# Kernel tuning notes

Hardware: AMD Instinct MI355X
Metric: run time of the kernel (lower is better)

Reference implementation:

```python
import jax, jax.numpy as jnp
import numpy as np

B, C, L = 1, 256, 1024      # batch, channels, seq_length
WIN, FEAT = 80, 256          # window_size, feature_size


def setup_inputs() -> dict:
    key = jax.random.key(0)
    ks = jax.random.split(key, 9)
    s = 0.02
    return {
        "x":  jax.random.normal(ks[0], (B, C, L), dtype=jnp.float32),
        # weights stored as [in, out] (transpose of torch Linear.weight)
        "Wq": jax.random.normal(ks[1], (WIN, FEAT), dtype=jnp.float32) * s,
        "bq": jax.random.normal(ks[2], (FEAT,), dtype=jnp.float32) * s,
        "Wk": jax.random.normal(ks[3], (WIN, FEAT), dtype=jnp.float32) * s,
        "bk": jax.random.normal(ks[4], (FEAT,), dtype=jnp.float32) * s,
        "Wv": jax.random.normal(ks[5], (WIN, FEAT), dtype=jnp.float32) * s,
        "bv": jax.random.normal(ks[6], (FEAT,), dtype=jnp.float32) * s,
        "Wf": jax.random.normal(ks[7], (FEAT, C), dtype=jnp.float32) * s,
        "bf": jax.random.normal(ks[8], (C,), dtype=jnp.float32) * s,
    }


def reference(x, Wq, bq, Wk, bk, Wv, bv, Wf, bf):
    Bb, Cc, Ll = x.shape
    half = WIN // 2
    # fixed-width window per position, clamped to stay in-bounds
    starts = jnp.clip(jnp.arange(Ll) - half, 0, Ll - WIN)          # [L]
    idx = starts[:, None] + jnp.arange(WIN)                        # [L, W]
    win = x[:, :, idx]                                             # [B, C, L, W]
    win = win.transpose(0, 2, 1, 3)                                # [B, L, C, W]
    q = win @ Wq + bq                                              # [B, L, C, F]
    k = win @ Wk + bk                                              # [B, L, C, F]
    v = win @ Wv + bv                                              # [B, L, C, F]
    scores = jax.nn.softmax(jnp.einsum('blcf,bldf->blcd', q, k), axis=-1)  # [B,L,C,C]
    attn = jnp.einsum('blcd,bldf->blcf', scores, v)                # [B, L, C, F]
    pooled = attn.mean(axis=2)                                     # [B, L, F] (mean over channels)
    out = pooled @ Wf + bf                                         # [B, L, C]
    return out.transpose(0, 2, 1)                                  # [B, C, L]
```

## Files before the change

### kernel.cpp

```cpp
#include <hip/hip_runtime.h>

#define Lc    1024
#define Cc    256
#define WINc  80
#define FEATc 256
#define RS    104
#define KP    96

typedef __attribute__((ext_vector_type(8))) short bf16x8;
typedef __attribute__((ext_vector_type(8))) unsigned short u16x8;
typedef __attribute__((ext_vector_type(4))) float f32x4;

__device__ inline unsigned short f2bf(float f) {
    unsigned int u = __float_as_uint(f);
    unsigned int r = u + 0x7FFFu + ((u >> 16) & 1u);
    return (unsigned short)(r >> 16);
}
__device__ inline float bf2f(unsigned short h) {
    return __uint_as_float(((unsigned int)h) << 16);
}

__global__ __launch_bounds__(128) void precompute_kernel(
    const float* __restrict__ Wq, const float* __restrict__ bq,
    const float* __restrict__ Wk,
    unsigned short* __restrict__ Gtb)
{
    const int t = blockIdx.x;
    const int w = threadIdx.x;
    if (w >= RS) return;
    float acc = 0.f;
    if (t < WINc && w < WINc) {
        for (int f = 0; f < FEATc; ++f)
            acc = fmaf(Wq[w * FEATc + f], Wk[t * FEATc + f], acc);
    } else if (t == WINc && w < WINc) {
        for (int f = 0; f < FEATc; ++f)
            acc = fmaf(bq[f], Wk[w * FEATc + f], acc);
    }
    Gtb[t * RS + w] = f2bf(acc);
}

__global__ __launch_bounds__(1024, 4) void local_attn_kernel(
    const float* __restrict__ x,
    const float* __restrict__ Wv, const float* __restrict__ bv,
    const float* __restrict__ Wf, const float* __restrict__ bf,
    const unsigned short* __restrict__ Gt_ws,
    float* __restrict__ out)
{
    __shared__ unsigned short winb[Cc * RS];
    __shared__ unsigned short Tb[Cc * RS];
    __shared__ unsigned short Gtb[KP * RS];
    __shared__ float sbeta[Cc];
    __shared__ float scratch[16 * Cc];
    __shared__ float sbar[Cc];
    __shared__ float ubuf[WINc];
    __shared__ float pooled[FEATc];

    const int l = blockIdx.x;
    int s = l - WINc / 2;
    s = s < 0 ? 0 : (s > (Lc - WINc) ? (Lc - WINc) : s);
    const int tid  = threadIdx.x;
    const int lane = tid & 63;
    const int wid  = tid >> 6;
    const int lr   = lane & 15;
    const int lkq  = lane >> 4;

    for (int i = tid; i < Cc * WINc / 8; i += 1024) {
        const int c  = i / 10;
        const int j8 = (i - c * 10) * 8;
        const float* xp = &x[c * Lc + s + j8];
        u16x8 v;
        #pragma unroll
        for (int e = 0; e < 8; ++e) v[e] = f2bf(xp[e]);
        *(u16x8*)&winb[c * RS + j8] = v;
    }
    for (int i = tid; i < Cc * 8; i += 1024) {
        const int c = i >> 3, j = i & 7;
        *(unsigned int*)&winb[c * RS + WINc + 2 * j] = 0u;
    }
    for (int i = tid; i < KP * RS / 2; i += 1024)
        ((unsigned int*)Gtb)[i] = ((const unsigned int*)Gt_ws)[i];
    __syncthreads();

    {
        const int arow = wid * 16 + lr;
        #pragma unroll
        for (int nt = 0; nt < 6; ++nt) {
            f32x4 acc = {0.f, 0.f, 0.f, 0.f};
            #pragma unroll
            for (int kc = 0; kc < 3; ++kc) {
                const int ko = kc * 32 + lkq * 8;
                bf16x8 a = *(const bf16x8*)&winb[arow * RS + ko];
                bf16x8 b = *(const bf16x8*)&Gtb[(nt * 16 + lr) * RS + ko];
                acc = __builtin_amdgcn_mfma_f32_16x16x32_bf16(a, b, acc, 0, 0, 0);
            }
            const int orow = wid * 16 + lkq * 4;
            const int ocol = nt * 16 + lr;
            #pragma unroll
            for (int r = 0; r < 4; ++r)
                Tb[(orow + r) * RS + ocol] = f2bf(acc[r]);
            if (nt == 5 && lr == 0) {
                #pragma unroll
                for (int r = 0; r < 4; ++r) sbeta[orow + r] = acc[r];
            }
        }
    }
    __syncthreads();

    f32x4 acc0[16];
    {
        const f32x4 z4 = {0.f, 0.f, 0.f, 0.f};
        #pragma unroll
        for (int nt = 0; nt < 16; ++nt) acc0[nt] = z4;
        const int rA = wid * 16 + lr;
        bf16x8 a0[3];
        #pragma unroll
        for (int kc = 0; kc < 3; ++kc)
            a0[kc] = *(const bf16x8*)&Tb[rA * RS + kc * 32 + lkq * 8];
        #pragma unroll
        for (int nt = 0; nt < 16; ++nt) {
            #pragma unroll
            for (int kc = 0; kc < 3; ++kc) {
                bf16x8 b = *(const bf16x8*)&winb[(nt * 16 + lr) * RS + kc * 32 + lkq * 8];
                acc0[nt] = __builtin_amdgcn_mfma_f32_16x16x32_bf16(a0[kc], b, acc0[nt], 0, 0, 0);
            }
        }
    }

    #pragma unroll
    for (int nt = 0; nt < 16; ++nt) {
        const float sb = sbeta[nt * 16 + lr];
        #pragma unroll
        for (int r = 0; r < 4; ++r) acc0[nt][r] += sb;
    }

    float rz[4];
    #pragma unroll
    for (int r = 0; r < 4; ++r) {
        float m = acc0[0][r];
        #pragma unroll
        for (int nt = 1; nt < 16; ++nt) m = fmaxf(m, acc0[nt][r]);
        m = fmaxf(m, __shfl_xor(m, 1));
        m = fmaxf(m, __shfl_xor(m, 2));
        m = fmaxf(m, __shfl_xor(m, 4));
        m = fmaxf(m, __shfl_xor(m, 8));
        float z = 0.f;
        #pragma unroll
        for (int nt = 0; nt < 16; ++nt) {
            const float e = __expf(acc0[nt][r] - m);
            acc0[nt][r] = e; z += e;
        }
        z += __shfl_xor(z, 1); z += __shfl_xor(z, 2);
        z += __shfl_xor(z, 4); z += __shfl_xor(z, 8);
        rz[r] = 1.f / z;
    }

    #pragma unroll
    for (int nt = 0; nt < 16; ++nt) {
        float v = 0.f;
        #pragma unroll
        for (int r = 0; r < 4; ++r) v = fmaf(acc0[nt][r], rz[r], v);
        v += __shfl_xor(v, 16);
        v += __shfl_xor(v, 32);
        if (lane < 16) scratch[wid * Cc + nt * 16 + lane] = v;
    }
    __syncthreads();

    if (tid < Cc) {
        float v = 0.f;
        #pragma unroll
        for (int w16 = 0; w16 < 16; ++w16) v += scratch[w16 * Cc + tid];
        sbar[tid] = v * (1.0f / Cc);
    }
    __syncthreads();

    if (tid < 8 * WINc) {
        const int w = tid % WINc;
        const int part = tid / WINc;
        float a = 0.f;
        for (int d = part * 32; d < part * 32 + 32; ++d)
            a = fmaf(sbar[d], bf2f(winb[d * RS + w]), a);
        scratch[part * WINc + w] = a;
    }
    __syncthreads();
    if (tid < WINc) {
        float v = 0.f;
        #pragma unroll
        for (int p = 0; p < 8; ++p) v += scratch[p * WINc + tid];
        ubuf[tid] = v;
    }
    __syncthreads();

    {
        const int f = tid & 255;
        const int part = tid >> 8;
        float a = 0.f;
        for (int w = part * 20; w < part * 20 + 20; ++w)
            a = fmaf(ubuf[w], Wv[w * FEATc + f], a);
        scratch[part * 256 + f] = a;
    }
    __syncthreads();
    if (tid < FEATc)
        pooled[tid] = scratch[tid] + scratch[256 + tid] +
                      scratch[512 + tid] + scratch[768 + tid] + bv[tid];
    __syncthreads();

    {
        const int co = tid & 255;
        const int part = tid >> 8;
        float a = 0.f;
        for (int f = part * 64; f < part * 64 + 64; ++f)
            a = fmaf(pooled[f], Wf[f * Cc + co], a);
        scratch[part * 256 + co] = a;
    }
    __syncthreads();
    if (tid < Cc)
        out[tid * Lc + l] = scratch[tid] + scratch[256 + tid] +
                            scratch[512 + tid] + scratch[768 + tid] + bf[tid];
}

extern "C" void kernel_launch(void* const* d_in, const int* in_sizes, int n_in,
                              void* d_out, int out_size, void* d_ws, size_t ws_size,
                              hipStream_t stream)
{
    const float* x  = (const float*)d_in[0];
    const float* Wq = (const float*)d_in[1];
    const float* bq = (const float*)d_in[2];
    const float* Wk = (const float*)d_in[3];
    const float* Wv = (const float*)d_in[5];
    const float* bv = (const float*)d_in[6];
    const float* Wf = (const float*)d_in[7];
    const float* bf = (const float*)d_in[8];
    float* out = (float*)d_out;

    unsigned short* Gtb = (unsigned short*)d_ws;

    hipLaunchKernelGGL(precompute_kernel, dim3(KP), dim3(128), 0, stream,
                       Wq, bq, Wk, Gtb);
    hipLaunchKernelGGL(local_attn_kernel, dim3(Lc), dim3(1024), 0, stream,
                       x, Wv, bv, Wf, bf, Gtb, out);
}
```

Baseline: 77.79 us.

## Fold Wv·Wf into precompute and use 32x32 MFMA register-resident scores

The precompute kernel now also folds Wv with Wf (scaled by 1/256) and bv·Wf+bf into a combined bias, so the main kernel does a single 80x256 matvec instead of two chained ones. The main kernel switches to 512 threads and 32x32x16 bf16 MFMAs. The intermediate T stays in registers as MFMA A-fragments instead of round-tripping through shared memory. Softmax drops the max subtraction, folds log2(e) into Gt and uses exp2. Skipping the max subtraction risks overflow when scores are large, and the reduced K padding and permuted slot order change the data layout.

```diff
diff --git a/kernel.cpp b/kernel.cpp
--- a/kernel.cpp
+++ b/kernel.cpp
@@ -3,219 +3,223 @@
 #define Lc    1024
 #define Cc    256
 #define WINc  80
-#define FEATc 256
-#define RS    104
-#define KP    96
-
-typedef __attribute__((ext_vector_type(8))) short bf16x8;
-typedef __attribute__((ext_vector_type(8))) unsigned short u16x8;
-typedef __attribute__((ext_vector_type(4))) float f32x4;
-
+#define SLOTS 96
+#define RS    88
+#define L2E   1.44269504088896340736f
+
+typedef __attribute__((ext_vector_type(8)))  short bf16x8;
+typedef __attribute__((ext_vector_type(16))) float f32x16;
+typedef __attribute__((ext_vector_type(4)))  unsigned int u32x4;
+
+__device__ inline float bf2f(unsigned short h) { return __uint_as_float(((unsigned int)h) << 16); }
+__device__ inline unsigned int cvt_pk_bf16(float lo, float hi) {
+    unsigned int r;
+    asm("v_cvt_pk_bf16_f32 %0, %1, %2" : "=v"(r) : "v"(lo), "v"(hi));
+    return r;
+}
 __device__ inline unsigned short f2bf(float f) {
     unsigned int u = __float_as_uint(f);
     unsigned int r = u + 0x7FFFu + ((u >> 16) & 1u);
     return (unsigned short)(r >> 16);
 }
-__device__ inline float bf2f(unsigned short h) {
-    return __uint_as_float(((unsigned int)h) << 16);
-}
-
-__global__ __launch_bounds__(128) void precompute_kernel(
+
+__global__ __launch_bounds__(256) void precompute_kernel(
     const float* __restrict__ Wq, const float* __restrict__ bq,
-    const float* __restrict__ Wk,
-    unsigned short* __restrict__ Gtb)
+    const float* __restrict__ Wk, const float* __restrict__ Wv,
+    const float* __restrict__ bv, const float* __restrict__ Wf,
+    const float* __restrict__ bf,
+    unsigned short* __restrict__ Gt, float* __restrict__ WvWf,
+    float* __restrict__ bias3)
 {
-    const int t = blockIdx.x;
-    const int w = threadIdx.x;
-    if (w >= RS) return;
-    float acc = 0.f;
-    if (t < WINc && w < WINc) {
-        for (int f = 0; f < FEATc; ++f)
-            acc = fmaf(Wq[w * FEATc + f], Wk[t * FEATc + f], acc);
-    } else if (t == WINc && w < WINc) {
-        for (int f = 0; f < FEATc; ++f)
-            acc = fmaf(bq[f], Wk[w * FEATc + f], acc);
-    }
-    Gtb[t * RS + w] = f2bf(acc);
-}
-
-__global__ __launch_bounds__(1024, 4) void local_attn_kernel(
+    const int b = blockIdx.x;
+    const int t = threadIdx.x;
+    if (b < SLOTS) {
+        if (t < WINc) {
+            const int s = b;
+            const int k = (s & ~12) | ((s & 4) << 1) | ((s & 8) >> 1);
+            float acc = 0.f;
+            if (k < WINc) {
+                for (int f = 0; f < 256; ++f)
+                    acc = fmaf(Wq[t * 256 + f], Wk[k * 256 + f], acc);
+            } else if (k == WINc) {
+                for (int f = 0; f < 256; ++f)
+                    acc = fmaf(bq[f], Wk[t * 256 + f], acc);
+            }
+            Gt[s * WINc + t] = (k <= WINc) ? f2bf(acc * L2E) : (unsigned short)0;
+        }
+    } else if (b < SLOTS + WINc) {
+        const int w = b - SLOTS;
+        float acc = 0.f;
+        for (int f = 0; f < 256; ++f)
+            acc = fmaf(Wv[w * 256 + f], Wf[f * 256 + t], acc);
+        WvWf[w * 256 + t] = acc * (1.0f / 256.0f);
+    } else {
+        float acc = bf[t];
+        for (int f = 0; f < 256; ++f)
+            acc = fmaf(bv[f], Wf[f * 256 + t], acc);
+        bias3[t] = acc;
+    }
+}
+
+__global__ __launch_bounds__(512, 2) void local_attn_kernel(
     const float* __restrict__ x,
-    const float* __restrict__ Wv, const float* __restrict__ bv,
-    const float* __restrict__ Wf, const float* __restrict__ bf,
     const unsigned short* __restrict__ Gt_ws,
+    const float* __restrict__ WvWf, const float* __restrict__ bias3,
     float* __restrict__ out)
 {
-    __shared__ unsigned short winb[Cc * RS];
-    __shared__ unsigned short Tb[Cc * RS];
-    __shared__ unsigned short Gtb[KP * RS];
+    __shared__ __align__(16) unsigned short winb[Cc * RS];
+    __shared__ __align__(16) unsigned short Gtb[SLOTS * RS];
     __shared__ float sbeta[Cc];
-    __shared__ float scratch[16 * Cc];
-    __shared__ float sbar[Cc];
+    __shared__ float sbarAcc[Cc];
     __shared__ float ubuf[WINc];
-    __shared__ float pooled[FEATc];
+    __shared__ float scratch[8 * Cc];
 
     const int l = blockIdx.x;
-    int s = l - WINc / 2;
-    s = s < 0 ? 0 : (s > (Lc - WINc) ? (Lc - WINc) : s);
+    int s0 = l - WINc / 2;
+    s0 = s0 < 0 ? 0 : (s0 > (Lc - WINc) ? (Lc - WINc) : s0);
     const int tid  = threadIdx.x;
     const int lane = tid & 63;
     const int wid  = tid >> 6;
-    const int lr   = lane & 15;
-    const int lkq  = lane >> 4;
-
-    for (int i = tid; i < Cc * WINc / 8; i += 1024) {
-        const int c  = i / 10;
-        const int j8 = (i - c * 10) * 8;
-        const float* xp = &x[c * Lc + s + j8];
-        u16x8 v;
-        #pragma unroll
-        for (int e = 0; e < 8; ++e) v[e] = f2bf(xp[e]);
-        *(u16x8*)&winb[c * RS + j8] = v;
-    }
-    for (int i = tid; i < Cc * 8; i += 1024) {
-        const int c = i >> 3, j = i & 7;
-        *(unsigned int*)&winb[c * RS + WINc + 2 * j] = 0u;
-    }
-    for (int i = tid; i < KP * RS / 2; i += 1024)
-        ((unsigned int*)Gtb)[i] = ((const unsigned int*)Gt_ws)[i];
-    __syncthreads();
-
+    const int ln31 = lane & 31;
+    const int hh   = lane >> 5;
+
+    for (int i = tid; i < Cc * WINc / 8; i += 512) {
+        const int c  = i & 255;
+        const int ch = i >> 8;
+        const float* xp = &x[c * Lc + s0 + ch * 8];
+        union { u32x4 u; bf16x8 v; } pk;
+        pk.u.x = cvt_pk_bf16(xp[0], xp[1]);
+        pk.u.y = cvt_pk_bf16(xp[2], xp[3]);
+        pk.u.z = cvt_pk_bf16(xp[4], xp[5]);
+        pk.u.w = cvt_pk_bf16(xp[6], xp[7]);
+        *(bf16x8*)&winb[c * RS + ch * 8] = pk.v;
+    }
+    for (int i = tid; i < SLOTS * WINc / 2; i += 512) {
+        const int s = i / 40;
+        const int j = i - s * 40;
+        ((unsigned int*)Gtb)[s * (RS / 2) + j] = ((const unsigned int*)Gt_ws)[i];
+    }
+    __syncthreads();
+
+    f32x16 tt[3];
     {
-        const int arow = wid * 16 + lr;
-        #pragma unroll
-        for (int nt = 0; nt < 6; ++nt) {
-            f32x4 acc = {0.f, 0.f, 0.f, 0.f};
+        bf16x8 bfr[5];
+        #pragma unroll
+        for (int t = 0; t < 5; ++t)
+            bfr[t] = *(const bf16x8*)&winb[(wid * 32 + ln31) * RS + t * 16 + hh * 8];
+        #pragma unroll
+        for (int mt = 0; mt < 3; ++mt) {
+            f32x16 a;
             #pragma unroll
-            for (int kc = 0; kc < 3; ++kc) {
-                const int ko = kc * 32 + lkq * 8;
-                bf16x8 a = *(const bf16x8*)&winb[arow * RS + ko];
-                bf16x8 b = *(const bf16x8*)&Gtb[(nt * 16 + lr) * RS + ko];
-                acc = __builtin_amdgcn_mfma_f32_16x16x32_bf16(a, b, acc, 0, 0, 0);
+            for (int r = 0; r < 16; ++r) a[r] = 0.f;
+            #pragma unroll
+            for (int t = 0; t < 5; ++t) {
+                bf16x8 afr = *(const bf16x8*)&Gtb[(mt * 32 + ln31) * RS + t * 16 + hh * 8];
+                a = __builtin_amdgcn_mfma_f32_32x32x16_bf16(afr, bfr[t], a, 0, 0, 0);
             }
-            const int orow = wid * 16 + lkq * 4;
-            const int ocol = nt * 16 + lr;
-            #pragma unroll
-            for (int r = 0; r < 4; ++r)
-                Tb[(orow + r) * RS + ocol] = f2bf(acc[r]);
-            if (nt == 5 && lr == 0) {
-                #pragma unroll
-                for (int r = 0; r < 4; ++r) sbeta[orow + r] = acc[r];
-            }
-        }
-    }
-    __syncthreads();
-
-    f32x4 acc0[16];
-    {
-        const f32x4 z4 = {0.f, 0.f, 0.f, 0.f};
-        #pragma unroll
-        for (int nt = 0; nt < 16; ++nt) acc0[nt] = z4;
-        const int rA = wid * 16 + lr;
-        bf16x8 a0[3];
-        #pragma unroll
-        for (int kc = 0; kc < 3; ++kc)
-            a0[kc] = *(const bf16x8*)&Tb[rA * RS + kc * 32 + lkq * 8];
-        #pragma unroll
-        for (int nt = 0; nt < 16; ++nt) {
-            #pragma unroll
-            for (int kc = 0; kc < 3; ++kc) {
-                bf16x8 b = *(const bf16x8*)&winb[(nt * 16 + lr) * RS + kc * 32 + lkq * 8];
-                acc0[nt] = __builtin_amdgcn_mfma_f32_16x16x32_bf16(a0[kc], b, acc0[nt], 0, 0, 0);
-            }
-        }
-    }
-
-    #pragma unroll
-    for (int nt = 0; nt < 16; ++nt) {
-        const float sb = sbeta[nt * 16 + lr];
-        #pragma unroll
-        for (int r = 0; r < 4; ++r) acc0[nt][r] += sb;
-    }
-
-    float rz[4];
-    #pragma unroll
-    for (int r = 0; r < 4; ++r) {
-        float m = acc0[0][r];
-        #pragma unroll
-        for (int nt = 1; nt < 16; ++nt) m = fmaxf(m, acc0[nt][r]);
-        m = fmaxf(m, __shfl_xor(m, 1));
-        m = fmaxf(m, __shfl_xor(m, 2));
-        m = fmaxf(m, __shfl_xor(m, 4));
-        m = fmaxf(m, __shfl_xor(m, 8));
-        float z = 0.f;
-        #pragma unroll
-        for (int nt = 0; nt < 16; ++nt) {
-            const float e = __expf(acc0[nt][r] - m);
-            acc0[nt][r] = e; z += e;
-        }
-        z += __shfl_xor(z, 1); z += __shfl_xor(z, 2);
-        z += __shfl_xor(z, 4); z += __shfl_xor(z, 8);
-        rz[r] = 1.f / z;
-    }
-
-    #pragma unroll
-    for (int nt = 0; nt < 16; ++nt) {
+            tt[mt] = a;
+        }
+    }
+    if (hh == 0) sbeta[wid * 32 + ln31] = tt[2][8];
+
+    bf16x8 af[5];
+    #pragma unroll
+    for (int t = 0; t < 5; ++t) {
+        const int m = t >> 1, o = 8 * (t & 1);
+        union { u32x4 u; bf16x8 v; } pk;
+        pk.u.x = cvt_pk_bf16(tt[m][o + 0], tt[m][o + 1]);
+        pk.u.y = cvt_pk_bf16(tt[m][o + 2], tt[m][o + 3]);
+        pk.u.z = cvt_pk_bf16(tt[m][o + 4], tt[m][o + 5]);
+        pk.u.w = cvt_pk_bf16(tt[m][o + 6], tt[m][o + 7]);
+        af[t] = pk.v;
+    }
+
+    f32x16 acc[8];
+    #pragma unroll
+    for (int nt = 0; nt < 8; ++nt) {
+        f32x16 a;
+        #pragma unroll
+        for (int r = 0; r < 16; ++r) a[r] = 0.f;
+        #pragma unroll
+        for (int t = 0; t < 5; ++t) {
+            bf16x8 b = *(const bf16x8*)&winb[(nt * 32 + ln31) * RS + t * 16 + hh * 8];
+            a = __builtin_amdgcn_mfma_f32_32x32x16_bf16(af[t], b, a, 0, 0, 0);
+        }
+        acc[nt] = a;
+    }
+    __syncthreads();
+
+    float zp[16];
+    #pragma unroll
+    for (int r = 0; r < 16; ++r) zp[r] = 0.f;
+    #pragma unroll
+    for (int nt = 0; nt < 8; ++nt) {
+        const float sb = sbeta[nt * 32 + ln31];
+        #pragma unroll
+        for (int r = 0; r < 16; ++r) {
+            const float e = exp2f(acc[nt][r] + sb);
+            acc[nt][r] = e;
+            zp[r] += e;
+        }
+    }
+    #pragma unroll
+    for (int r = 0; r < 16; ++r) {
+        float z = zp[r];
+        z += __shfl_xor(z, 1);
+        z += __shfl_xor(z, 2);
+        z += __shfl_xor(z, 4);
+        z += __shfl_xor(z, 8);
+        z += __shfl_xor(z, 16);
+        zp[r] = __builtin_amdgcn_rcpf(z);
+    }
+
+    #pragma unroll
+    for (int nt = 0; nt < 8; ++nt) {
         float v = 0.f;
         #pragma unroll
-        for (int r = 0; r < 4; ++r) v = fmaf(acc0[nt][r], rz[r], v);
-        v += __shfl_xor(v, 16);
+        for (int r = 0; r < 16; ++r) v = fmaf(acc[nt][r], zp[r], v);
         v += __shfl_xor(v, 32);
-        if (lane < 16) scratch[wid * Cc + nt * 16 + lane] = v;
+        if (lane < 32) scratch[wid * Cc + nt * 32 + ln31] = v;
     }
     __syncthreads();
 
     if (tid < Cc) {
         float v = 0.f;
         #pragma unroll
-        for (int w16 = 0; w16 < 16; ++w16) v += scratch[w16 * Cc + tid];
-        sbar[tid] = v * (1.0f / Cc);
-    }
-    __syncthreads();
-
-    if (tid < 8 * WINc) {
+        for (int w8 = 0; w8 < 8; ++w8) v += scratch[w8 * Cc + tid];
+        sbarAcc[tid] = v;
+    }
+    __syncthreads();
+
+    if (tid < 4 * WINc) {
         const int w = tid % WINc;
         const int part = tid / WINc;
+        const int d0 = part * 64;
         float a = 0.f;
-        for (int d = part * 32; d < part * 32 + 32; ++d)
-            a = fmaf(sbar[d], bf2f(winb[d * RS + w]), a);
+        #pragma unroll 8
+        for (int d = d0; d < d0 + 64; ++d)
+            a = fmaf(sbarAcc[d], bf2f(winb[d * RS + w]), a);
         scratch[part * WINc + w] = a;
     }
     __syncthreads();
-    if (tid < WINc) {
-        float v = 0.f;
-        #pragma unroll
-        for (int p = 0; p < 8; ++p) v += scratch[p * WINc + tid];
-        ubuf[tid] = v;
-    }
-    __syncthreads();
-
-    {
-        const int f = tid & 255;
-        const int part = tid >> 8;
-        float a = 0.f;
-        for (int w = part * 20; w < part * 20 + 20; ++w)
-            a = fmaf(ubuf[w], Wv[w * FEATc + f], a);
-        scratch[part * 256 + f] = a;
-    }
-    __syncthreads();
-    if (tid < FEATc)
-        pooled[tid] = scratch[tid] + scratch[256 + tid] +
-                      scratch[512 + tid] + scratch[768 + tid] + bv[tid];
+    if (tid < WINc)
+        ubuf[tid] = scratch[tid] + scratch[WINc + tid] +
+                    scratch[2 * WINc + tid] + scratch[3 * WINc + tid];
     __syncthreads();
 
     {
         const int co = tid & 255;
         const int part = tid >> 8;
+        const int w0 = part * 40;
         float a = 0.f;
-        for (int f = part * 64; f < part * 64 + 64; ++f)
-            a = fmaf(pooled[f], Wf[f * Cc + co], a);
+        #pragma unroll 8
+        for (int w = w0; w < w0 + 40; ++w)
+            a = fmaf(ubuf[w], WvWf[w * 256 + co], a);
         scratch[part * 256 + co] = a;
     }
     __syncthreads();
     if (tid < Cc)
-        out[tid * Lc + l] = scratch[tid] + scratch[256 + tid] +
-                            scratch[512 + tid] + scratch[768 + tid] + bf[tid];
+        out[tid * Lc + l] = scratch[tid] + scratch[256 + tid] + bias3[tid];
 }
 
 extern "C" void kernel_launch(void* const* d_in, const int* in_sizes, int n_in,
@@ -232,10 +236,12 @@
     const float* bf = (const float*)d_in[8];
     float* out = (float*)d_out;
 
-    unsigned short* Gtb = (unsigned short*)d_ws;
-
-    hipLaunchKernelGGL(precompute_kernel, dim3(KP), dim3(128), 0, stream,
-                       Wq, bq, Wk, Gtb);
-    hipLaunchKernelGGL(local_attn_kernel, dim3(Lc), dim3(1024), 0, stream,
-                       x, Wv, bv, Wf, bf, Gtb, out);
-}
+    unsigned short* Gt = (unsigned short*)d_ws;
+    float* WvWf  = (float*)((char*)d_ws + SLOTS * WINc * 2);
+    float* bias3 = WvWf + WINc * 256;
+
+    hipLaunchKernelGGL(precompute_kernel, dim3(SLOTS + WINc + 1), dim3(256), 0, stream,
+                       Wq, bq, Wk, Wv, bv, Wf, bf, Gt, WvWf, bias3);
+    hipLaunchKernelGGL(local_attn_kernel, dim3(Lc), dim3(512), 0, stream,
+                       x, Gt, WvWf, bias3, out);
+}
```

New measurement: 72.08 us. -7.3%, faster.
